# Performance work log

Measured on AMD Instinct MI355X. Metric: run time of the kernel, lower is better.

## Reference

```python
import jax, jax.numpy as jnp
import numpy as np
import math

IN_FEATURES = 729   # n^2 with n = 27 = 3^3
HIDDEN = 2916
OUT_FEATURES = 729
BASE = 3
FACTOR = 0
B, D = 64, 768      # batch, channel dim (x: [B, D, IN_FEATURES])


def _butterfly_factor_to_matrix(twiddle, factor_index):
    # twiddle: (n//b, b, b) -> dense n x n butterfly factor matrix (numpy, setup-time only)
    n_div_b, b, _ = twiddle.shape
    n = b * n_div_b
    stride = b ** factor_index
    # eye(n) rearranged: 'bs (diagblk j stride)' -> (bs, diagblk, j, stride)
    x = np.eye(n, dtype=np.float32).reshape(n, n // (b * stride), b, stride)
    # twiddle rearranged: '(diagblk stride) i j' -> (diagblk, stride, i, j)
    t = twiddle.reshape(n // (b * stride), stride, b, b)
    out = np.einsum('dsij,bdjs->bdis', t, x).reshape(n, n)
    return out.T


def _sparse_mask():
    b = BASE
    log_b_n = int(math.log(math.sqrt(IN_FEATURES), b))
    n = b ** log_b_n
    twiddle = np.arange(1, n * b + 1, dtype=np.float32).reshape(n // b, b, b)
    m1 = _butterfly_factor_to_matrix(twiddle, FACTOR)
    mask = np.kron(m1, m1)
    return jnp.asarray((mask > 0).astype(np.float32))  # [729, 729] 0/1 mask


def setup_inputs() -> dict:
    key = jax.random.key(0)
    k1, k2, k3, k4 = jax.random.split(key, 4)
    x = jax.random.normal(k1, (B, D, IN_FEATURES), jnp.float32)
    w1 = jax.random.normal(k2, (HIDDEN, IN_FEATURES), jnp.float32) / math.sqrt(IN_FEATURES)
    w2 = jax.random.normal(k3, (OUT_FEATURES, HIDDEN), jnp.float32) / math.sqrt(HIDDEN)
    b2 = jax.random.normal(k4, (OUT_FEATURES,), jnp.float32) * 0.01
    return {"x": x, "w1": w1, "w2": w2, "b2": b2, "sparse_mask": _sparse_mask()}


def reference(x, w1, w2, b2, sparse_mask):
    # attn_s[s,t] = sum_d fc1.W[d,s] * fc2.W[t,d], then butterfly-masked
    attn = jnp.einsum('ds,td->st', w1, w2) * sparse_mask  # [in, out]
    out = jnp.einsum('bds,st->bdt', x, attn) + b2          # [B, D, out]
    return jax.nn.gelu(out, approximate=False)             # torch nn.GELU uses exact erf
```

## Files before the change

kernel.cpp:

```cpp
#include <hip/hip_runtime.h>
#include <hip/hip_bf16.h>


__device__ __forceinline__ float gelu_f(float v) {
    float u2 = v * v;
    float z = -1.5957691216f * v * fmaf(0.044715f, u2, 1.0f);
    float e = __expf(z);
    return v * __builtin_amdgcn_rcpf(1.0f + e);
}

__global__ void attn_zero_kernel(float* __restrict__ attn) {
    int i = blockIdx.x * 256 + threadIdx.x;
    if (i < 81 * 81) attn[i] = 0.0f;
}

#define CH 108

__global__ __launch_bounds__(256) void bfly_attn_kernel(
        const float* __restrict__ w1,
        const float* __restrict__ w2,
        float* __restrict__ attn)
{
    const int G1    = blockIdx.x % 9;
    const int d0    = (blockIdx.x / 9) * CH;
    const int tid   = threadIdx.x;

    __shared__ float ws1[CH * 81];
    __shared__ float ws2[81 * CH];

    for (int i = tid; i < CH * 81; i += 256) {
        int dl = i / 81, c = i % 81;
        ws1[i] = w1[(d0 + dl) * 729 + 81 * G1 + c];
    }
    for (int i = tid; i < 81 * CH; i += 256) {
        int tl = i / CH, dl = i % CH;
        ws2[i] = w2[(81 * G1 + tl) * 2916 + d0 + dl];
    }
    __syncthreads();

    if (tid < 243) {
        const int G2  = tid / 27;
        const int ls  = (tid % 27) / 3;
        const int lt0 = (tid % 3) * 3;
        const int s_l = 27 * (ls / 3) + 3 * G2 + (ls % 3);
        int t_l[3];
        #pragma unroll
        for (int j = 0; j < 3; ++j) {
            int lt = lt0 + j;
            t_l[j] = 27 * (lt / 3) + 3 * G2 + (lt % 3);
        }

        float a0 = 0.f, a1 = 0.f, a2 = 0.f;
        for (int dl = 0; dl < CH; ++dl) {
            float av = ws1[dl * 81 + s_l];
            a0 = fmaf(av, ws2[t_l[0] * CH + dl], a0);
            a1 = fmaf(av, ws2[t_l[1] * CH + dl], a1);
            a2 = fmaf(av, ws2[t_l[2] * CH + dl], a2);
        }

        const int g = 9 * G1 + G2;
        float* dst = &attn[g * 81 + ls * 9 + lt0];
        atomicAdd(dst + 0, a0);
        atomicAdd(dst + 1, a1);
        atomicAdd(dst + 2, a2);
    }
}

#define ROWS 8

__global__ __launch_bounds__(256) void bfly_mlp_kernel(
        const float* __restrict__ xg,
        const float* __restrict__ attn,
        const float* __restrict__ b2g,
        float* __restrict__ outg)
{
    __shared__ float xs[ROWS * 729];

    const int tid = threadIdx.x;
    const long long rowbase = (long long)blockIdx.x * ROWS;

    float a[9][3], bias[3];
    int tb = 0, sb = 0;
    const bool active = (tid < 243);
    if (active) {
        const int t1 = tid / 9;
        const int G2 = tid % 9;
        const int G1 = t1 / 3;
        const int li = t1 % 3;
        tb = 27 * t1 + 3 * G2;
        sb = 81 * G1 + 3 * G2;
        const int g  = 9 * G1 + G2;
        #pragma unroll
        for (int ls = 0; ls < 9; ++ls)
            #pragma unroll
            for (int j = 0; j < 3; ++j)
                a[ls][j] = attn[g * 81 + ls * 9 + 3 * li + j];
        #pragma unroll
        for (int j = 0; j < 3; ++j) bias[j] = b2g[tb + j];
    }

    {
        const uint4* src = (const uint4*)(xg + rowbase * 729);
        uint4* dst = (uint4*)xs;
        for (int i = tid; i < (ROWS * 729) / 4; i += 256) dst[i] = src[i];
    }
    __syncthreads();

    if (active) {
        #pragma unroll 2
        for (int r = 0; r < ROWS; ++r) {
            const int xb = r * 729 + sb;
            float xv[9];
            #pragma unroll
            for (int i2 = 0; i2 < 3; ++i2)
                #pragma unroll
                for (int j2 = 0; j2 < 3; ++j2)
                    xv[3*i2 + j2] = xs[xb + 27*i2 + j2];

            float acc0 = bias[0], acc1 = bias[1], acc2 = bias[2];
            #pragma unroll
            for (int ls = 0; ls < 9; ++ls) {
                acc0 = fmaf(xv[ls], a[ls][0], acc0);
                acc1 = fmaf(xv[ls], a[ls][1], acc1);
                acc2 = fmaf(xv[ls], a[ls][2], acc2);
            }

            const long long ob = (rowbase + r) * 729 + tb;
            outg[ob + 0] = gelu_f(acc0);
            outg[ob + 1] = gelu_f(acc1);
            outg[ob + 2] = gelu_f(acc2);
        }
    }
}

extern "C" void kernel_launch(void* const* d_in, const int* in_sizes, int n_in,
                              void* d_out, int out_size, void* d_ws, size_t ws_size,
                              hipStream_t stream) {
    const float* x  = (const float*)d_in[0];
    const float* w1 = (const float*)d_in[1];
    const float* w2 = (const float*)d_in[2];
    const float* b2 = (const float*)d_in[3];

    float* attn = (float*)d_ws;

    attn_zero_kernel<<<26, 256, 0, stream>>>(attn);
    bfly_attn_kernel<<<9 * 27, 256, 0, stream>>>(w1, w2, attn);

    const int n_rows = 64 * 768;
    bfly_mlp_kernel<<<n_rows / ROWS, 256, 0, stream>>>(
        x, attn, b2, (float*)d_out);
}
```

Measured before the change: 282.3 us.

## Pipeline MLP kernel with double-buffered direct-to-LDS loads and deferred nontemporal stores

The MLP kernel now runs a persistent-style loop over 8 tiles of 4 rows per block. Each next tile is staged into a second LDS buffer with global_load_lds while the current tile is computed. Output stores are deferred one iteration, made nontemporal, and tb is simplified to 3*tid, which gives contiguous coalesced writes. Together these aim to overlap HBM reads with compute and to avoid cache pollution from the write stream, at the cost of more registers (res array, launch_bounds occupancy hint) and fewer blocks.

```diff
diff --git a/kernel.cpp b/kernel.cpp
--- a/kernel.cpp
+++ b/kernel.cpp
@@ -66,28 +66,29 @@
     }
 }
 
-#define ROWS 8
+#define ROWS 4
+#define TPB  8
+#define NBLK 1536
 
-__global__ __launch_bounds__(256) void bfly_mlp_kernel(
+__global__ __launch_bounds__(256, 6) void bfly_mlp_kernel(
         const float* __restrict__ xg,
         const float* __restrict__ attn,
         const float* __restrict__ b2g,
         float* __restrict__ outg)
 {
-    __shared__ float xs[ROWS * 729];
+    __shared__ float xs[2][ROWS * 729];
 
     const int tid = threadIdx.x;
-    const long long rowbase = (long long)blockIdx.x * ROWS;
+    const bool active = (tid < 243);
 
     float a[9][3], bias[3];
     int tb = 0, sb = 0;
-    const bool active = (tid < 243);
     if (active) {
         const int t1 = tid / 9;
         const int G2 = tid % 9;
         const int G1 = t1 / 3;
         const int li = t1 % 3;
-        tb = 27 * t1 + 3 * G2;
+        tb = 3 * tid;
         sb = 81 * G1 + 3 * G2;
         const int g  = 9 * G1 + G2;
         #pragma unroll
@@ -99,36 +100,79 @@
         for (int j = 0; j < 3; ++j) bias[j] = b2g[tb + j];
     }
 
-    {
-        const uint4* src = (const uint4*)(xg + rowbase * 729);
-        uint4* dst = (uint4*)xs;
-        for (int i = tid; i < (ROWS * 729) / 4; i += 256) dst[i] = src[i];
+    const long long row0 = (long long)blockIdx.x * (ROWS * TPB);
+
+    auto stage = [&](int t, int buf) {
+        const uint4* __restrict__ src =
+            (const uint4*)(xg + (row0 + (long long)t * ROWS) * 729);
+        #pragma unroll
+        for (int k = 0; k < 3; ++k) {
+            const int i = tid + k * 256;
+            if (i < 729) {
+                __builtin_amdgcn_global_load_lds(
+                    (const __attribute__((address_space(1))) void*)(src + i),
+                    (__attribute__((address_space(3))) void*)(&xs[buf][i * 4]),
+                    16, 0, 0);
+            }
+        }
+    };
+
+    int cur = 0;
+    stage(0, 0);
+
+    float res[ROWS][3];
+
+    for (int t = 0; t < TPB; ++t) {
+        asm volatile("s_waitcnt vmcnt(0)" ::: "memory");
+        __builtin_amdgcn_s_barrier();
+        asm volatile("" ::: "memory");
+
+        if (t + 1 < TPB) stage(t + 1, cur ^ 1);
+
+        if (active) {
+            if (t > 0) {
+                const long long rb = (row0 + (long long)(t - 1) * ROWS) * 729 + tb;
+                #pragma unroll
+                for (int r = 0; r < ROWS; ++r) {
+                    __builtin_nontemporal_store(res[r][0], &outg[rb + r * 729 + 0]);
+                    __builtin_nontemporal_store(res[r][1], &outg[rb + r * 729 + 1]);
+                    __builtin_nontemporal_store(res[r][2], &outg[rb + r * 729 + 2]);
+                }
+            }
+
+            const float* xb = &xs[cur][0];
+            #pragma unroll
+            for (int r = 0; r < ROWS; ++r) {
+                const float* xr = xb + r * 729 + sb;
+                float xv[9];
+                #pragma unroll
+                for (int i2 = 0; i2 < 3; ++i2)
+                    #pragma unroll
+                    for (int j2 = 0; j2 < 3; ++j2)
+                        xv[3 * i2 + j2] = xr[27 * i2 + j2];
+
+                float acc0 = bias[0], acc1 = bias[1], acc2 = bias[2];
+                #pragma unroll
+                for (int ls = 0; ls < 9; ++ls) {
+                    acc0 = fmaf(xv[ls], a[ls][0], acc0);
+                    acc1 = fmaf(xv[ls], a[ls][1], acc1);
+                    acc2 = fmaf(xv[ls], a[ls][2], acc2);
+                }
+                res[r][0] = gelu_f(acc0);
+                res[r][1] = gelu_f(acc1);
+                res[r][2] = gelu_f(acc2);
+            }
+        }
+        cur ^= 1;
     }
-    __syncthreads();
 
     if (active) {
-        #pragma unroll 2
+        const long long rb = (row0 + (long long)(TPB - 1) * ROWS) * 729 + tb;
+        #pragma unroll
         for (int r = 0; r < ROWS; ++r) {
-            const int xb = r * 729 + sb;
-            float xv[9];
-            #pragma unroll
-            for (int i2 = 0; i2 < 3; ++i2)
-                #pragma unroll
-                for (int j2 = 0; j2 < 3; ++j2)
-                    xv[3*i2 + j2] = xs[xb + 27*i2 + j2];
-
-            float acc0 = bias[0], acc1 = bias[1], acc2 = bias[2];
-            #pragma unroll
-            for (int ls = 0; ls < 9; ++ls) {
-                acc0 = fmaf(xv[ls], a[ls][0], acc0);
-                acc1 = fmaf(xv[ls], a[ls][1], acc1);
-                acc2 = fmaf(xv[ls], a[ls][2], acc2);
-            }
-
-            const long long ob = (rowbase + r) * 729 + tb;
-            outg[ob + 0] = gelu_f(acc0);
-            outg[ob + 1] = gelu_f(acc1);
-            outg[ob + 2] = gelu_f(acc2);
+            __builtin_nontemporal_store(res[r][0], &outg[rb + r * 729 + 0]);
+            __builtin_nontemporal_store(res[r][1], &outg[rb + r * 729 + 1]);
+            __builtin_nontemporal_store(res[r][2], &outg[rb + r * 729 + 2]);
         }
     }
 }
@@ -146,7 +190,5 @@
     attn_zero_kernel<<<26, 256, 0, stream>>>(attn);
     bfly_attn_kernel<<<9 * 27, 256, 0, stream>>>(w1, w2, attn);
 
-    const int n_rows = 64 * 768;
-    bfly_mlp_kernel<<<n_rows / ROWS, 256, 0, stream>>>(
-        x, attn, b2, (float*)d_out);
+    bfly_mlp_kernel<<<NBLK, 256, 0, stream>>>(x, attn, b2, (float*)d_out);
 }
```

Result: slower. 441.9 us (+56.5%).
